# Kernel optimization log

Hardware: AMD Instinct MI355X
Metric: run time of the kernel (lower is better)

## Reference

```python
import jax, jax.numpy as jnp
import numpy as np

B, E, F1, F2, C = 8192, 8, 1024, 2048, 100


def setup_inputs() -> dict:
    key = jax.random.key(0)
    k = jax.random.split(key, 6)
    s1 = 1.0 / np.sqrt(F1)
    s2 = 1.0 / np.sqrt(F2)
    return {
        "domain": jax.random.randint(k[0], (B,), 0, E, dtype=jnp.int32),
        "x": jax.random.normal(k[1], (B, F1), dtype=jnp.float32),
        "W1": jax.random.normal(k[2], (E, F1, F2), dtype=jnp.float32) * s1,
        "b1": jax.random.normal(k[3], (E, F2), dtype=jnp.float32) * s1,
        "W2": jax.random.normal(k[4], (E, F2, C), dtype=jnp.float32) * s2,
        "b2": jax.random.normal(k[5], (E, C), dtype=jnp.float32) * s2,
    }


def reference(domain, x, W1, b1, W2, b2):
    # All-experts 2-layer MLP over the full batch (faithful to the torch loop,
    # expressed as batched einsums over the expert axis e).
    h = jax.nn.relu(jnp.einsum("bf,efh->beh", x, W1) + b1[None, :, :])  # [B,E,F2]
    logits = jnp.einsum("beh,ehc->bec", h, W2) + b2[None, :, :]          # [B,E,C]
    # Gather the expert selected by each sample's domain index.
    sel = jnp.take_along_axis(logits, domain[:, None, None].astype(jnp.int32), axis=1)
    sel = sel[:, 0, :]                                                    # [B,C]
    return jax.nn.softmax(sel, axis=-1)
```

## Files before the change

### kernel.cpp

```cpp
#include <hip/hip_runtime.h>
#include <math.h>

#define NB 8192
#define NE 8
#define F1 1024
#define F2 2048
#define NC 100
#define NCP 112
#define TM 128
#define BK 64
#define NCC (F2 / 128)
#define MAXTY 72

#define WS_COUNTS 0
#define WS_OFF 8
#define WS_CUR 17
#define WS_ROWS 64

#define OFF_XH  ((size_t)65536)
#define SZ_X    ((size_t)NB * F1)
#define OFF_W1H (OFF_XH + 4 * SZ_X)
#define SZ_W1   ((size_t)NE * F2 * F1)
#define OFF_W2H (OFF_W1H + 4 * SZ_W1)
#define SZ_W2   ((size_t)NE * NCP * F2)

typedef float f32x4 __attribute__((ext_vector_type(4)));
typedef short s16x8 __attribute__((ext_vector_type(8)));
typedef unsigned short u16x8 __attribute__((ext_vector_type(8)));
typedef unsigned short u16x4 __attribute__((ext_vector_type(4)));

__device__ __forceinline__ unsigned short bf_hi(float f) {
    unsigned u = __float_as_uint(f);
    return (unsigned short)((u + 0x7FFFu + ((u >> 16) & 1u)) >> 16);
}
__device__ __forceinline__ float bf_up(unsigned short h) {
    return __uint_as_float(((unsigned)h) << 16);
}

typedef const __attribute__((address_space(1))) unsigned cgu;
typedef __attribute__((address_space(3))) unsigned ldu;
__device__ __forceinline__ void gl16(const void* g, void* l) {
    __builtin_amdgcn_global_load_lds((cgu*)g, (ldu*)l, 16, 0, 0);
}

__global__ void k_hist(const int* __restrict__ dom, int* ws) {
    int b = blockIdx.x * 256 + threadIdx.x;
    if (b < NB) atomicAdd(&ws[WS_COUNTS + dom[b]], 1);
}

__global__ void k_scan(int* ws) {
    if (threadIdx.x != 0 || blockIdx.x != 0) return;
    ws[WS_OFF + 0] = 0;
    for (int e = 0; e < NE; ++e) {
        ws[WS_OFF + e + 1] = ws[WS_OFF + e] + ws[WS_COUNTS + e];
        ws[WS_CUR + e] = ws[WS_OFF + e];
    }
}

__global__ void k_scatter(const int* __restrict__ dom, int* ws) {
    int b = blockIdx.x * 256 + threadIdx.x;
    if (b < NB) {
        int p = atomicAdd(&ws[WS_CUR + dom[b]], 1);
        ws[WS_ROWS + p] = b;
    }
}

__global__ void k_split_x(const float* __restrict__ x, unsigned short* __restrict__ xh) {
    unsigned short* xl = xh + SZ_X;
    size_t i = (size_t)blockIdx.x * 256 + threadIdx.x;
    float4 v = *(const float4*)(x + i * 4);
    u16x4 h, l;
    float f[4] = {v.x, v.y, v.z, v.w};
#pragma unroll
    for (int t = 0; t < 4; ++t) {
        unsigned short hh = bf_hi(f[t]);
        h[t] = hh;
        l[t] = bf_hi(f[t] - bf_up(hh));
    }
    *(u16x4*)(xh + i * 4) = h;
    *(u16x4*)(xl + i * 4) = l;
}

__global__ void k_split_w1t(const float* __restrict__ W1, unsigned short* __restrict__ w1h) {
    unsigned short* w1l = w1h + SZ_W1;
    __shared__ float t[64][68];
    const int e = blockIdx.z, k0 = blockIdx.y * 64, n0 = blockIdx.x * 64;
    const float* src = W1 + ((size_t)e * F1 + k0) * F2 + n0;
#pragma unroll
    for (int i = 0; i < 4; ++i) {
        int u = threadIdx.x + 256 * i;
        int k = u >> 4, n4 = (u & 15) * 4;
        float4 v = *(const float4*)(src + (size_t)k * F2 + n4);
        t[k][n4] = v.x; t[k][n4 + 1] = v.y; t[k][n4 + 2] = v.z; t[k][n4 + 3] = v.w;
    }
    __syncthreads();
#pragma unroll
    for (int i = 0; i < 2; ++i) {
        int u = threadIdx.x + 256 * i;
        int n = u >> 3, kg = u & 7;
        u16x8 hv, lv;
#pragma unroll
        for (int j = 0; j < 8; ++j) {
            float v = t[kg * 8 + j][n];
            unsigned short hh = bf_hi(v);
            hv[j] = hh;
            lv[j] = bf_hi(v - bf_up(hh));
        }
        size_t dst = ((size_t)e * F2 + n0 + n) * F1 + k0 + kg * 8;
        *(u16x8*)(w1h + dst) = hv;
        *(u16x8*)(w1l + dst) = lv;
    }
}

__global__ void k_split_w2t(const float* __restrict__ W2, unsigned short* __restrict__ w2h) {
    unsigned short* w2l = w2h + SZ_W2;
    __shared__ float t[64][NC + 4];
    const int e = blockIdx.y, k0 = blockIdx.x * 64;
    const float* src = W2 + ((size_t)e * F2 + k0) * NC;
    for (int u = threadIdx.x; u < 64 * NC; u += 256) {
        int k = u / NC, c = u - k * NC;
        t[k][c] = src[u];
    }
    __syncthreads();
#pragma unroll
    for (int i = 0; i < 4; ++i) {
        int u = threadIdx.x + 256 * i;
        if (u < NCP * 8) {
            int c = u >> 3, kg = u & 7;
            u16x8 hv, lv;
#pragma unroll
            for (int j = 0; j < 8; ++j) {
                float v = (c < NC) ? t[kg * 8 + j][c] : 0.f;
                unsigned short hh = bf_hi(v);
                hv[j] = hh;
                lv[j] = bf_hi(v - bf_up(hh));
            }
            size_t dst = ((size_t)e * NCP + c) * F2 + k0 + kg * 8;
            *(u16x8*)(w2h + dst) = hv;
            *(u16x8*)(w2l + dst) = lv;
        }
    }
}

__global__ __launch_bounds__(256, 2) void k_g1(
    const int* __restrict__ ws, const unsigned short* __restrict__ xh,
    const unsigned short* __restrict__ w1h, const unsigned short* __restrict__ w2h,
    const float* __restrict__ b1, float* __restrict__ out)
{
    __shared__ __align__(16) unsigned short sb[32768];
    __shared__ int rows[TM];
    __shared__ int hdr[3];
    const int tid = threadIdx.x;
    const int cc = blockIdx.x;

    if (tid == 0) {
        int ty = blockIdx.y, acc0 = 0, e = -1, t = 0;
        for (int i = 0; i < NE; ++i) {
            int te = (ws[WS_COUNTS + i] + TM - 1) / TM;
            if (ty < acc0 + te) { e = i; t = ty - acc0; break; }
            acc0 += te;
        }
        hdr[0] = e;
        if (e >= 0) {
            hdr[1] = min(TM, ws[WS_COUNTS + e] - t * TM);
            hdr[2] = ws[WS_OFF + e] + t * TM;
        }
    }
    __syncthreads();
    const int e = hdr[0];
    if (e < 0) return;
    const int nr = hdr[1];
    if (tid < TM) rows[tid] = ws[WS_ROWS + hdr[2] + min(tid, nr - 1)];
    __syncthreads();

    const int wave = tid >> 6, lane = tid & 63;
    const int wm = wave >> 1, wn = wave & 1;
    const int lg = lane >> 4, ln = lane & 15;
    const int l7 = ln & 7;

    const unsigned short* pA[4];
    const unsigned short* pB[4];
#pragma unroll
    for (int i = 0; i < 4; ++i) {
        int u = tid + 256 * i;
        int r = u >> 3, g = u & 7;
        pA[i] = xh + (size_t)rows[r] * F1 + (g ^ (r & 7)) * 8;
        pB[i] = w1h + ((size_t)e * F2 + cc * 128 + r) * F1 + ((g ^ (r & 7)) * 8);
    }

    float bias[4];
#pragma unroll
    for (int nf = 0; nf < 4; ++nf)
        bias[nf] = b1[e * F2 + cc * 128 + wn * 64 + nf * 16 + ln];

    f32x4 acc[4][4];
#pragma unroll
    for (int m = 0; m < 4; ++m)
#pragma unroll
        for (int n = 0; n < 4; ++n) acc[m][n] = (f32x4){0.f, 0.f, 0.f, 0.f};

    const int wb = wave * 512;
    for (int kt = 0; kt < F1 / BK; ++kt) {
        const int k0 = kt * BK;
#pragma unroll
        for (int i = 0; i < 4; ++i) {
            gl16(pA[i] + k0,          &sb[wb + i * 2048]);
            gl16(pA[i] + SZ_X + k0,   &sb[8192 + wb + i * 2048]);
            gl16(pB[i] + k0,          &sb[16384 + wb + i * 2048]);
            gl16(pB[i] + SZ_W1 + k0,  &sb[24576 + wb + i * 2048]);
        }
        __syncthreads();
#pragma unroll
        for (int kk = 0; kk < 2; ++kk) {
            const int sz = (kk * 4 + lg) ^ l7;
            s16x8 ah[4], al[4];
#pragma unroll
            for (int m = 0; m < 4; ++m) {
                int off = (wm * 64 + m * 16 + ln) * 64 + sz * 8;
                ah[m] = *(const s16x8*)&sb[off];
                al[m] = *(const s16x8*)&sb[8192 + off];
            }
#pragma unroll
            for (int n = 0; n < 4; ++n) {
                int off = (wn * 64 + n * 16 + ln) * 64 + sz * 8;
                s16x8 bh = *(const s16x8*)&sb[16384 + off];
                s16x8 bl = *(const s16x8*)&sb[24576 + off];
#pragma unroll
                for (int m = 0; m < 4; ++m) {
                    acc[m][n] = __builtin_amdgcn_mfma_f32_16x16x32_bf16(ah[m], bh, acc[m][n], 0, 0, 0);
                    acc[m][n] = __builtin_amdgcn_mfma_f32_16x16x32_bf16(al[m], bh, acc[m][n], 0, 0, 0);
                    acc[m][n] = __builtin_amdgcn_mfma_f32_16x16x32_bf16(ah[m], bl, acc[m][n], 0, 0, 0);
                }
            }
        }
        __syncthreads();
    }

    f32x4 acc2[2][7];
#pragma unroll
    for (int mf = 0; mf < 2; ++mf)
#pragma unroll
        for (int cf = 0; cf < 7; ++cf) acc2[mf][cf] = (f32x4){0.f, 0.f, 0.f, 0.f};

#pragma unroll
    for (int s = 0; s < 2; ++s) {
        __syncthreads();
        if (wn == s) {
#pragma unroll
            for (int m = 0; m < 4; ++m)
#pragma unroll
                for (int nf = 0; nf < 4; ++nf) {
                    const float bb = bias[nf];
                    const int k2 = nf * 16 + ln;
#pragma unroll
                    for (int reg = 0; reg < 4; ++reg) {
                        int row = wm * 64 + m * 16 + lg * 4 + reg;
                        float v = fmaxf(acc[m][nf][reg] + bb, 0.f);
                        unsigned short hh = bf_hi(v);
                        int off = row * 64 + ((k2 >> 3) ^ (row & 7)) * 8 + (k2 & 7);
                        sb[off] = hh;
                        sb[8192 + off] = bf_hi(v - bf_up(hh));
                    }
                }
        }
        for (int ch = wave; ch < 14; ch += 4) {
            int u = ch * 64 + lane;
            int c = u >> 3, g = u & 7;
            const unsigned short* src =
                w2h + ((size_t)e * NCP + c) * F2 + cc * 128 + s * 64 + ((g ^ (c & 7)) * 8);
            gl16(src,         &sb[16384 + ch * 512]);
            gl16(src + SZ_W2, &sb[24576 + ch * 512]);
        }
        __syncthreads();
#pragma unroll
        for (int kk = 0; kk < 2; ++kk) {
            const int sz = (kk * 4 + lg) ^ l7;
            s16x8 hh[2], hl[2];
#pragma unroll
            for (int mf = 0; mf < 2; ++mf) {
                int off = (wave * 32 + mf * 16 + ln) * 64 + sz * 8;
                hh[mf] = *(const s16x8*)&sb[off];
                hl[mf] = *(const s16x8*)&sb[8192 + off];
            }
#pragma unroll
            for (int cf = 0; cf < 7; ++cf) {
                int off = (cf * 16 + ln) * 64 + sz * 8;
                s16x8 wh = *(const s16x8*)&sb[16384 + off];
                s16x8 wl = *(const s16x8*)&sb[24576 + off];
#pragma unroll
                for (int mf = 0; mf < 2; ++mf) {
                    acc2[mf][cf] = __builtin_amdgcn_mfma_f32_16x16x32_bf16(hh[mf], wh, acc2[mf][cf], 0, 0, 0);
                    acc2[mf][cf] = __builtin_amdgcn_mfma_f32_16x16x32_bf16(hl[mf], wh, acc2[mf][cf], 0, 0, 0);
                    acc2[mf][cf] = __builtin_amdgcn_mfma_f32_16x16x32_bf16(hh[mf], wl, acc2[mf][cf], 0, 0, 0);
                }
            }
        }
    }

#pragma unroll
    for (int mf = 0; mf < 2; ++mf)
#pragma unroll
        for (int cf = 0; cf < 7; ++cf)
#pragma unroll
            for (int reg = 0; reg < 4; ++reg) {
                int row = wave * 32 + mf * 16 + lg * 4 + reg;
                int c = cf * 16 + ln;
                if (row < nr && c < NC)
                    atomicAdd(out + (size_t)rows[row] * NC + c, acc2[mf][cf][reg]);
            }
}

__global__ void k_sm(const int* __restrict__ dom, const float* __restrict__ b2,
                     float* __restrict__ out)
{
    const int row = blockIdx.x * 4 + (threadIdx.x >> 6);
    const int lane = threadIdx.x & 63;
    const int e = dom[row];
    float* base = out + (size_t)row * NC;
    float v0 = base[lane] + b2[e * NC + lane];
    float v1 = -1e30f;
    if (lane + 64 < NC) v1 = base[lane + 64] + b2[e * NC + lane + 64];
    float m = fmaxf(v0, v1);
#pragma unroll
    for (int s = 1; s < 64; s <<= 1) m = fmaxf(m, __shfl_xor(m, s));
    float p0 = expf(v0 - m);
    float p1 = (lane + 64 < NC) ? expf(v1 - m) : 0.f;
    float sum = p0 + p1;
#pragma unroll
    for (int s = 1; s < 64; s <<= 1) sum += __shfl_xor(sum, s);
    float inv = 1.f / sum;
    base[lane] = p0 * inv;
    if (lane + 64 < NC) base[lane + 64] = p1 * inv;
}

extern "C" void kernel_launch(void* const* d_in, const int* in_sizes, int n_in,
                              void* d_out, int out_size, void* d_ws, size_t ws_size,
                              hipStream_t stream)
{
    const int*   dom = (const int*)d_in[0];
    const float* x   = (const float*)d_in[1];
    const float* W1  = (const float*)d_in[2];
    const float* b1  = (const float*)d_in[3];
    const float* W2  = (const float*)d_in[4];
    const float* b2  = (const float*)d_in[5];
    float*       out = (float*)d_out;
    int*         ws  = (int*)d_ws;

    unsigned short* xh  = (unsigned short*)((char*)d_ws + OFF_XH);
    unsigned short* w1h = (unsigned short*)((char*)d_ws + OFF_W1H);
    unsigned short* w2h = (unsigned short*)((char*)d_ws + OFF_W2H);

    hipMemsetAsync(ws, 0, 64 * sizeof(int), stream);
    hipMemsetAsync(out, 0, (size_t)NB * NC * sizeof(float), stream);
    hipLaunchKernelGGL(k_hist,     dim3(NB / 256), dim3(256), 0, stream, dom, ws);
    hipLaunchKernelGGL(k_scan,     dim3(1), dim3(1), 0, stream, ws);
    hipLaunchKernelGGL(k_scatter,  dim3(NB / 256), dim3(256), 0, stream, dom, ws);
    hipLaunchKernelGGL(k_split_x,  dim3(NB * F1 / 1024), dim3(256), 0, stream, x, xh);
    hipLaunchKernelGGL(k_split_w1t, dim3(F2 / 64, F1 / 64, NE), dim3(256), 0, stream, W1, w1h);
    hipLaunchKernelGGL(k_split_w2t, dim3(F2 / 64, NE), dim3(256), 0, stream, W2, w2h);
    hipLaunchKernelGGL(k_g1,       dim3(NCC, MAXTY), dim3(256), 0, stream,
                       ws, xh, w1h, w2h, b1, out);
    hipLaunchKernelGGL(k_sm,       dim3(NB / 4), dim3(256), 0, stream, dom, b2, out);
}
```

Baseline: 426.3 us.

## Double-buffer GEMM K-loop and fuse routing histogram/scan into one plan kernel

```diff
diff --git a/kernel.cpp b/kernel.cpp
--- a/kernel.cpp
+++ b/kernel.cpp
@@ -8,14 +8,16 @@
 #define NC 100
 #define NCP 112
 #define TM 128
-#define BK 64
+#define BK 32
+#define NKT (F1 / BK)
 #define NCC (F2 / 128)
 #define MAXTY 72
 
-#define WS_COUNTS 0
-#define WS_OFF 8
-#define WS_CUR 17
-#define WS_ROWS 64
+#define WS_CUR   17
+#define WS_TYE   32
+#define WS_TYR   104
+#define WS_TYN   176
+#define WS_ROWS  256
 
 #define OFF_XH  ((size_t)65536)
 #define SZ_X    ((size_t)NB * F1)
@@ -43,47 +45,82 @@
     __builtin_amdgcn_global_load_lds((cgu*)g, (ldu*)l, 16, 0, 0);
 }
 
-__global__ void k_hist(const int* __restrict__ dom, int* ws) {
-    int b = blockIdx.x * 256 + threadIdx.x;
-    if (b < NB) atomicAdd(&ws[WS_COUNTS + dom[b]], 1);
-}
-
-__global__ void k_scan(int* ws) {
-    if (threadIdx.x != 0 || blockIdx.x != 0) return;
-    ws[WS_OFF + 0] = 0;
-    for (int e = 0; e < NE; ++e) {
-        ws[WS_OFF + e + 1] = ws[WS_OFF + e] + ws[WS_COUNTS + e];
-        ws[WS_CUR + e] = ws[WS_OFF + e];
-    }
-}
-
-__global__ void k_scatter(const int* __restrict__ dom, int* ws) {
-    int b = blockIdx.x * 256 + threadIdx.x;
-    if (b < NB) {
-        int p = atomicAdd(&ws[WS_CUR + dom[b]], 1);
-        ws[WS_ROWS + p] = b;
-    }
+__global__ __launch_bounds__(512) void k_plan(const int* __restrict__ dom, int* ws) {
+    __shared__ int wh[8][8];
+    const int tid = threadIdx.x, wave = tid >> 6, lane = tid & 63;
+    int cnt[NE];
+#pragma unroll
+    for (int e = 0; e < NE; ++e) cnt[e] = 0;
+    for (int i = tid; i < NB / 4; i += 512) {
+        int4 d = ((const int4*)dom)[i];
+        int v[4] = {d.x, d.y, d.z, d.w};
+#pragma unroll
+        for (int t = 0; t < 4; ++t)
+#pragma unroll
+            for (int e = 0; e < NE; ++e)
+                cnt[e] += (int)__popcll(__ballot(v[t] == e));
+    }
+    if (lane == 0)
+#pragma unroll
+        for (int e = 0; e < NE; ++e) wh[wave][e] = cnt[e];
+    __syncthreads();
+    if (tid == 0) {
+        int c[NE], off = 0, ty = 0;
+        for (int e = 0; e < NE; ++e) {
+            c[e] = 0;
+            for (int w = 0; w < 8; ++w) c[e] += wh[w][e];
+        }
+        for (int e = 0; e < NE; ++e) {
+            ws[WS_CUR + e] = off;
+            int nt = (c[e] + TM - 1) / TM;
+            for (int t = 0; t < nt; ++t) {
+                ws[WS_TYE + ty] = e;
+                ws[WS_TYR + ty] = off + t * TM;
+                ws[WS_TYN + ty] = min(TM, c[e] - t * TM);
+                ++ty;
+            }
+            off += c[e];
+        }
+        for (; ty < MAXTY; ++ty) ws[WS_TYN + ty] = 0;
+    }
+}
+
+__global__ __launch_bounds__(256) void k_scatter(const int* __restrict__ dom, int* ws) {
+    __shared__ int lh[NE], base[NE];
+    const int tid = threadIdx.x;
+    if (tid < NE) lh[tid] = 0;
+    __syncthreads();
+    const int b = blockIdx.x * 256 + tid;
+    const int e = dom[b];
+    const int r = atomicAdd(&lh[e], 1);
+    __syncthreads();
+    if (tid < NE) base[tid] = atomicAdd(&ws[WS_CUR + tid], lh[tid]);
+    __syncthreads();
+    ws[WS_ROWS + base[e] + r] = b;
 }
 
 __global__ void k_split_x(const float* __restrict__ x, unsigned short* __restrict__ xh) {
     unsigned short* xl = xh + SZ_X;
-    size_t i = (size_t)blockIdx.x * 256 + threadIdx.x;
-    float4 v = *(const float4*)(x + i * 4);
-    u16x4 h, l;
-    float f[4] = {v.x, v.y, v.z, v.w};
-#pragma unroll
-    for (int t = 0; t < 4; ++t) {
-        unsigned short hh = bf_hi(f[t]);
-        h[t] = hh;
-        l[t] = bf_hi(f[t] - bf_up(hh));
-    }
-    *(u16x4*)(xh + i * 4) = h;
-    *(u16x4*)(xl + i * 4) = l;
+#pragma unroll
+    for (int q = 0; q < 4; ++q) {
+        size_t i = (size_t)blockIdx.x * 1024 + q * 256 + threadIdx.x;
+        float4 v = *(const float4*)(x + i * 4);
+        u16x4 h, l;
+        float f[4] = {v.x, v.y, v.z, v.w};
+#pragma unroll
+        for (int t = 0; t < 4; ++t) {
+            unsigned short hh = bf_hi(f[t]);
+            h[t] = hh;
+            l[t] = bf_hi(f[t] - bf_up(hh));
+        }
+        *(u16x4*)(xh + i * 4) = h;
+        *(u16x4*)(xl + i * 4) = l;
+    }
 }
 
 __global__ void k_split_w1t(const float* __restrict__ W1, unsigned short* __restrict__ w1h) {
     unsigned short* w1l = w1h + SZ_W1;
-    __shared__ float t[64][68];
+    __shared__ float t[64][65];
     const int e = blockIdx.z, k0 = blockIdx.y * 64, n0 = blockIdx.x * 64;
     const float* src = W1 + ((size_t)e * F1 + k0) * F2 + n0;
 #pragma unroll
@@ -114,7 +151,7 @@
 
 __global__ void k_split_w2t(const float* __restrict__ W2, unsigned short* __restrict__ w2h) {
     unsigned short* w2l = w2h + SZ_W2;
-    __shared__ float t[64][NC + 4];
+    __shared__ float t[64][NC + 1];
     const int e = blockIdx.y, k0 = blockIdx.x * 64;
     const float* src = W2 + ((size_t)e * F2 + k0) * NC;
     for (int u = threadIdx.x; u < 64 * NC; u += 256) {
@@ -149,28 +186,15 @@
 {
     __shared__ __align__(16) unsigned short sb[32768];
     __shared__ int rows[TM];
-    __shared__ int hdr[3];
     const int tid = threadIdx.x;
     const int cc = blockIdx.x;
-
-    if (tid == 0) {
-        int ty = blockIdx.y, acc0 = 0, e = -1, t = 0;
-        for (int i = 0; i < NE; ++i) {
-            int te = (ws[WS_COUNTS + i] + TM - 1) / TM;
-            if (ty < acc0 + te) { e = i; t = ty - acc0; break; }
-            acc0 += te;
-        }
-        hdr[0] = e;
-        if (e >= 0) {
-            hdr[1] = min(TM, ws[WS_COUNTS + e] - t * TM);
-            hdr[2] = ws[WS_OFF + e] + t * TM;
-        }
-    }
-    __syncthreads();
-    const int e = hdr[0];
-    if (e < 0) return;
-    const int nr = hdr[1];
-    if (tid < TM) rows[tid] = ws[WS_ROWS + hdr[2] + min(tid, nr - 1)];
+    const int ty = blockIdx.y;
+
+    const int nr = ws[WS_TYN + ty];
+    if (nr <= 0) return;
+    const int e = ws[WS_TYE + ty];
+    const int rbase = ws[WS_TYR + ty];
+    if (tid < TM) rows[tid] = ws[WS_ROWS + rbase + min(tid, nr - 1)];
     __syncthreads();
 
     const int wave = tid >> 6, lane = tid & 63;
@@ -178,15 +202,17 @@
     const int lg = lane >> 4, ln = lane & 15;
     const int l7 = ln & 7;
 
-    const unsigned short* pA[4];
-    const unsigned short* pB[4];
-#pragma unroll
-    for (int i = 0; i < 4; ++i) {
+    const unsigned short* pA[2];
+    const unsigned short* pB[2];
+#pragma unroll
+    for (int i = 0; i < 2; ++i) {
         int u = tid + 256 * i;
-        int r = u >> 3, g = u & 7;
-        pA[i] = xh + (size_t)rows[r] * F1 + (g ^ (r & 7)) * 8;
-        pB[i] = w1h + ((size_t)e * F2 + cc * 128 + r) * F1 + ((g ^ (r & 7)) * 8);
-    }
+        int r = u >> 2, s = u & 3, g = s ^ (r & 3);
+        pA[i] = xh + (size_t)rows[r] * F1 + g * 8;
+        pB[i] = w1h + ((size_t)e * F2 + cc * 128 + r) * F1 + g * 8;
+    }
+    const int ldst0 = tid * 8;
+    const int ldst1 = ldst0 + 2048;
 
     float bias[4];
 #pragma unroll
@@ -199,42 +225,57 @@
 #pragma unroll
         for (int n = 0; n < 4; ++n) acc[m][n] = (f32x4){0.f, 0.f, 0.f, 0.f};
 
-    const int wb = wave * 512;
-    for (int kt = 0; kt < F1 / BK; ++kt) {
-        const int k0 = kt * BK;
-#pragma unroll
-        for (int i = 0; i < 4; ++i) {
-            gl16(pA[i] + k0,          &sb[wb + i * 2048]);
-            gl16(pA[i] + SZ_X + k0,   &sb[8192 + wb + i * 2048]);
-            gl16(pB[i] + k0,          &sb[16384 + wb + i * 2048]);
-            gl16(pB[i] + SZ_W1 + k0,  &sb[24576 + wb + i * 2048]);
-        }
-        __syncthreads();
-#pragma unroll
-        for (int kk = 0; kk < 2; ++kk) {
-            const int sz = (kk * 4 + lg) ^ l7;
-            s16x8 ah[4], al[4];
+#define STAGE(kt, db)                                                          \
+    {                                                                          \
+        const int ko = (kt) * BK;                                              \
+        const int b0 = (db) * 16384;                                           \
+        gl16(pA[0] + ko,         &sb[b0 + ldst0]);                             \
+        gl16(pA[1] + ko,         &sb[b0 + ldst1]);                             \
+        gl16(pA[0] + SZ_X + ko,  &sb[b0 + 4096 + ldst0]);                      \
+        gl16(pA[1] + SZ_X + ko,  &sb[b0 + 4096 + ldst1]);                      \
+        gl16(pB[0] + ko,         &sb[b0 + 8192 + ldst0]);                      \
+        gl16(pB[1] + ko,         &sb[b0 + 8192 + ldst1]);                      \
+        gl16(pB[0] + SZ_W1 + ko, &sb[b0 + 12288 + ldst0]);                     \
+        gl16(pB[1] + SZ_W1 + ko, &sb[b0 + 12288 + ldst1]);                     \
+    }
+
+    STAGE(0, 0);
+    for (int kt = 0; kt < NKT; ++kt) {
+        const int cur = kt & 1;
+        if (kt + 1 < NKT) {
+            STAGE(kt + 1, cur ^ 1);
+            asm volatile("s_waitcnt vmcnt(8)" ::: "memory");
+        } else {
+            asm volatile("s_waitcnt vmcnt(0)" ::: "memory");
+        }
+        __builtin_amdgcn_s_barrier();
+        __builtin_amdgcn_sched_barrier(0);
+        const int b0 = cur * 16384;
+        s16x8 ah[4], al[4];
+#pragma unroll
+        for (int m = 0; m < 4; ++m) {
+            int r = wm * 64 + m * 16 + ln;
+            int off = b0 + r * 32 + (lg ^ (r & 3)) * 8;
+            ah[m] = *(const s16x8*)&sb[off];
+            al[m] = *(const s16x8*)&sb[4096 + off];
+        }
+#pragma unroll
+        for (int n = 0; n < 4; ++n) {
+            int r = wn * 64 + n * 16 + ln;
+            int off = b0 + 8192 + r * 32 + (lg ^ (r & 3)) * 8;
+            s16x8 bh = *(const s16x8*)&sb[off];
+            s16x8 bl = *(const s16x8*)&sb[4096 + off];
 #pragma unroll
             for (int m = 0; m < 4; ++m) {
-                int off = (wm * 64 + m * 16 + ln) * 64 + sz * 8;
-                ah[m] = *(const s16x8*)&sb[off];
-                al[m] = *(const s16x8*)&sb[8192 + off];
-            }
-#pragma unroll
-            for (int n = 0; n < 4; ++n) {
-                int off = (wn * 64 + n * 16 + ln) * 64 + sz * 8;
-                s16x8 bh = *(const s16x8*)&sb[16384 + off];
-                s16x8 bl = *(const s16x8*)&sb[24576 + off];
-#pragma unroll
-                for (int m = 0; m < 4; ++m) {
-                    acc[m][n] = __builtin_amdgcn_mfma_f32_16x16x32_bf16(ah[m], bh, acc[m][n], 0, 0, 0);
-                    acc[m][n] = __builtin_amdgcn_mfma_f32_16x16x32_bf16(al[m], bh, acc[m][n], 0, 0, 0);
-                    acc[m][n] = __builtin_amdgcn_mfma_f32_16x16x32_bf16(ah[m], bl, acc[m][n], 0, 0, 0);
-                }
-            }
-        }
-        __syncthreads();
-    }
+                acc[m][n] = __builtin_amdgcn_mfma_f32_16x16x32_bf16(ah[m], bh, acc[m][n], 0, 0, 0);
+                acc[m][n] = __builtin_amdgcn_mfma_f32_16x16x32_bf16(al[m], bh, acc[m][n], 0, 0, 0);
+                acc[m][n] = __builtin_amdgcn_mfma_f32_16x16x32_bf16(ah[m], bl, acc[m][n], 0, 0, 0);
+            }
+        }
+        __builtin_amdgcn_sched_barrier(0);
+        __builtin_amdgcn_s_barrier();
+    }
+#undef STAGE
 
     f32x4 acc2[2][7];
 #pragma unroll
@@ -350,15 +391,13 @@
     unsigned short* w1h = (unsigned short*)((char*)d_ws + OFF_W1H);
     unsigned short* w2h = (unsigned short*)((char*)d_ws + OFF_W2H);
 
-    hipMemsetAsync(ws, 0, 64 * sizeof(int), stream);
     hipMemsetAsync(out, 0, (size_t)NB * NC * sizeof(float), stream);
-    hipLaunchKernelGGL(k_hist,     dim3(NB / 256), dim3(256), 0, stream, dom, ws);
-    hipLaunchKernelGGL(k_scan,     dim3(1), dim3(1), 0, stream, ws);
-    hipLaunchKernelGGL(k_scatter,  dim3(NB / 256), dim3(256), 0, stream, dom, ws);
-    hipLaunchKernelGGL(k_split_x,  dim3(NB * F1 / 1024), dim3(256), 0, stream, x, xh);
+    hipLaunchKernelGGL(k_plan,      dim3(1), dim3(512), 0, stream, dom, ws);
+    hipLaunchKernelGGL(k_scatter,   dim3(NB / 256), dim3(256), 0, stream, dom, ws);
+    hipLaunchKernelGGL(k_split_x,   dim3(NB * F1 / 4096), dim3(256), 0, stream, x, xh);
     hipLaunchKernelGGL(k_split_w1t, dim3(F2 / 64, F1 / 64, NE), dim3(256), 0, stream, W1, w1h);
     hipLaunchKernelGGL(k_split_w2t, dim3(F2 / 64, NE), dim3(256), 0, stream, W2, w2h);
-    hipLaunchKernelGGL(k_g1,       dim3(NCC, MAXTY), dim3(256), 0, stream,
+    hipLaunchKernelGGL(k_g1,        dim3(NCC, MAXTY), dim3(256), 0, stream,
                        ws, xh, w1h, w2h, b1, out);
-    hipLaunchKernelGGL(k_sm,       dim3(NB / 4), dim3(256), 0, stream, dom, b2, out);
-}
+    hipLaunchKernelGGL(k_sm,        dim3(NB / 4), dim3(256), 0, stream, dom, b2, out);
+}
```

New measurement: 384.8 us. 9.7% less time.
